# Optimization experiments

Hardware: AMD Instinct MI355X
Metric: run time of the kernel (lower is better)

## Reference

```python
import jax, jax.numpy as jnp
import numpy as np

N, E, HID, HEADS, EDIM = 32768, 262144, 64, 4, 3
C = HID  # per-head out channels (concat=False -> mean over heads)


def setup_inputs() -> dict:
    key = jax.random.key(0)
    ks = jax.random.split(key, 24)
    g = lambda k, shape, s=1.0: jax.random.normal(k, shape, jnp.float32) * s
    s_lin = 1.0 / np.sqrt(HID)
    s_edge = 1.0 / np.sqrt(EDIM)
    s_att = 1.0 / np.sqrt(C)
    inp = {
        "t": jnp.zeros((1,), jnp.float32),
        "h": g(ks[0], (N, HID)),
        "edge_index": jax.random.randint(ks[1], (2, E), 0, N, jnp.int32),
        "edge_attr": g(ks[2], (E, EDIM)),
        "W1": g(ks[3], (HID, HEADS * C), s_lin),
        "We1": g(ks[4], (EDIM, HEADS * C), s_edge),
        "att_src1": g(ks[5], (HEADS, C), s_att),
        "att_dst1": g(ks[6], (HEADS, C), s_att),
        "att_edge1": g(ks[7], (HEADS, C), s_att),
        "b1": jnp.zeros((C,), jnp.float32),
        "ln_g1": jnp.ones((HID,), jnp.float32),
        "ln_b1": jnp.zeros((HID,), jnp.float32),
        # last GAT layer's lin weight is scaled by 0.1 in __init__
        "W2": g(ks[8], (HID, HEADS * C), s_lin) * 0.1,
        "We2": g(ks[9], (EDIM, HEADS * C), s_edge),
        "att_src2": g(ks[10], (HEADS, C), s_att),
        "att_dst2": g(ks[11], (HEADS, C), s_att),
        "att_edge2": g(ks[12], (HEADS, C), s_att),
        "b2": jnp.zeros((C,), jnp.float32),
        "ln_g2": jnp.ones((HID,), jnp.float32),
        "ln_b2": jnp.zeros((HID,), jnp.float32),
    }
    return inp


def _gat_layer(z, src, dst, edge_attr, W, We, a_src, a_dst, a_edge, b):
    # PyG GATConv(edge_dim>0, concat=False, add_self_loops=False), eval mode (no dropout)
    x = (z @ W).reshape(-1, HEADS, C)                      # [N,H,C]
    alpha_s = jnp.einsum("nhc,hc->nh", x, a_src)           # [N,H]
    alpha_d = jnp.einsum("nhc,hc->nh", x, a_dst)           # [N,H]
    e = (edge_attr @ We).reshape(-1, HEADS, C)             # [E,H,C]
    alpha_e = jnp.einsum("ehc,hc->eh", e, a_edge)          # [E,H]
    logit = jax.nn.leaky_relu(alpha_s[src] + alpha_d[dst] + alpha_e, 0.2)  # [E,H]
    # segment softmax over incoming edges of each destination node
    m = jax.lax.stop_gradient(jax.ops.segment_max(logit, dst, num_segments=N))
    ex = jnp.exp(logit - m[dst])
    denom = jax.ops.segment_sum(ex, dst, num_segments=N)
    alpha = ex / (denom[dst] + 1e-16)                      # [E,H]
    msg = x[src] * alpha[..., None]                        # [E,H,C] gather + weight
    out = jax.ops.segment_sum(msg, dst, num_segments=N)    # [N,H,C] scatter-add
    return out.mean(axis=1) + b                            # head mean + bias -> [N,C]


def _layernorm(x, g, b, eps=1e-5):
    mu = x.mean(-1, keepdims=True)
    var = ((x - mu) ** 2).mean(-1, keepdims=True)
    return (x - mu) * jax.lax.rsqrt(var + eps) * g + b


def reference(t, h, edge_index, edge_attr, W1, We1, att_src1, att_dst1, att_edge1, b1,
              ln_g1, ln_b1, W2, We2, att_src2, att_dst2, att_edge2, b2, ln_g2, ln_b2):
    del t  # autonomous ODE func: t unused
    src, dst = edge_index[0], edge_index[1]
    z = h
    z = jax.nn.silu(_layernorm(_gat_layer(z, src, dst, edge_attr, W1, We1, att_src1, att_dst1, att_edge1, b1), ln_g1, ln_b1))
    z = jax.nn.silu(_layernorm(_gat_layer(z, src, dst, edge_attr, W2, We2, att_src2, att_dst2, att_edge2, b2), ln_g2, ln_b2))
    return z
```

## Files before the change

kernel.cpp:

```cpp
#include <hip/hip_runtime.h>
#include <math.h>

#define HIDDEN 64
#define HEADS 4
#define HC 256
#define CAP 64

typedef __attribute__((ext_vector_type(8))) short short8;
typedef __attribute__((ext_vector_type(4))) float f32x4;

__device__ __forceinline__ unsigned short f2bf(float f) {
    unsigned int u = __float_as_uint(f);
    u += 0x7fffu + ((u >> 16) & 1u);
    return (unsigned short)(u >> 16);
}

__global__ __launch_bounds__(256) void k_fused(const int* __restrict__ dst,
                                               const int* __restrict__ src,
                                               const float* __restrict__ ea,
                                               const float* __restrict__ h,
                                               const float* __restrict__ W1f,
                                               const float* __restrict__ W2f,
                                               const float* __restrict__ We1,
                                               const float* __restrict__ at1,
                                               const float* __restrict__ We2,
                                               const float* __restrict__ at2,
                                               int* __restrict__ counts,
                                               int* __restrict__ sb,
                                               float* __restrict__ eab,
                                               ushort* __restrict__ zb,
                                               ushort* __restrict__ wt1,
                                               ushort* __restrict__ wt2,
                                               float* __restrict__ wr, int E) {
    int t = threadIdx.x, b = blockIdx.x;
    if (b < 1024) {
        int e = b * 256 + t;
        if (e < E) {
            int d = dst[e];
            int c = atomicAdd(&counts[d], 1);
            if (c < CAP) {
                size_t slot = (size_t)d * CAP + c;
                sb[slot] = src[e];
                *(float4*)&eab[slot * 4] =
                    make_float4(ea[e * 3 + 0], ea[e * 3 + 1], ea[e * 3 + 2], 0.f);
            }
        }
    } else if (b < 3072) {
        int i = (b - 1024) * 256 + t;
        float4 v = ((const float4*)h)[i];
        ushort4 o;
        o.x = f2bf(v.x); o.y = f2bf(v.y); o.z = f2bf(v.z); o.w = f2bf(v.w);
        ((ushort4*)zb)[i] = o;
    } else if (b < 3136) {
        int j = (b - 3072) * 256 + t;
        int c = j >> 6, k = j & 63;
        wt1[j] = f2bf(W1f[k * HC + c]);
        wt2[j] = f2bf(W2f[k * HC + c]);
    } else {
        int wv = t >> 6, lane = t & 63;
#pragma unroll
        for (int it = 0; it < 6; ++it) {
            int comb = wv + it * 4;
            int layer = comb / 12;
            int dh = comb % 12;
            int d = dh >> 2, hh = dh & 3;
            const float* We = layer ? We2 : We1;
            const float* at = layer ? at2 : at1;
            float v = We[d * HC + hh * HIDDEN + lane] * at[hh * HIDDEN + lane];
            for (int o = 32; o > 0; o >>= 1) v += __shfl_down(v, o);
            if (lane == 0) wr[layer * 16 + d * HEADS + hh] = v;
        }
    }
}

__global__ __launch_bounds__(256) void k_tmfma(const ushort* __restrict__ zb,
                                               const ushort* __restrict__ wt,
                                               const float* __restrict__ asw,
                                               const float* __restrict__ adw,
                                               ushort* __restrict__ xb,
                                               float* __restrict__ as_,
                                               float* __restrict__ ad_) {
    int wave = threadIdx.x >> 6, lane = threadIdx.x & 63;
    int q = lane & 15, quad = lane >> 4;
    int row0 = blockIdx.x * 64 + wave * 16;

    const ushort* zrow = zb + (size_t)(row0 + q) * 64 + quad * 8;
    short8 a0 = *(const short8*)(zrow);
    short8 a1 = *(const short8*)(zrow + 32);

#pragma unroll
    for (int h = 0; h < 4; ++h) {
        float vs[4] = {0.f, 0.f, 0.f, 0.f};
        float vd[4] = {0.f, 0.f, 0.f, 0.f};
#pragma unroll
        for (int nt = 0; nt < 4; ++nt) {
            int col0 = h * 64 + nt * 16;
            const ushort* wrow = wt + (size_t)(col0 + q) * 64 + quad * 8;
            short8 b0 = *(const short8*)(wrow);
            short8 b1 = *(const short8*)(wrow + 32);
            f32x4 acc = {0.f, 0.f, 0.f, 0.f};
            acc = __builtin_amdgcn_mfma_f32_16x16x32_bf16(a0, b0, acc, 0, 0, 0);
            acc = __builtin_amdgcn_mfma_f32_16x16x32_bf16(a1, b1, acc, 0, 0, 0);
            int c = col0 + q;
            float aw = asw[c], dw = adw[c];
#pragma unroll
            for (int r = 0; r < 4; ++r) {
                float v = acc[r];
                xb[(size_t)(row0 + quad * 4 + r) * HC + c] = f2bf(v);
                vs[r] += v * aw;
                vd[r] += v * dw;
            }
        }
#pragma unroll
        for (int o = 1; o < 16; o <<= 1) {
#pragma unroll
            for (int r = 0; r < 4; ++r) {
                vs[r] += __shfl_xor(vs[r], o);
                vd[r] += __shfl_xor(vd[r], o);
            }
        }
        if (q < 4) {
            int n = row0 + quad * 4 + q;
            as_[n * 4 + h] = vs[q];
            ad_[n * 4 + h] = vd[q];
        }
    }
}

__global__ __launch_bounds__(256) void k_aggregate(
        const ushort* __restrict__ xb, const float* __restrict__ eab,
        const int* __restrict__ sb, const int* __restrict__ counts,
        const float* __restrict__ as_, const float* __restrict__ ad_,
        const float* __restrict__ wrl,
        const float* __restrict__ bias, const float* __restrict__ lng,
        const float* __restrict__ lnb, float* __restrict__ outf,
        ushort* __restrict__ outb, int N) {
    int lane = threadIdx.x & 63;
    int h = lane >> 4, sub = lane & 15;
    int e = sub & 1, g = sub >> 1;
    int wid = blockIdx.x * 4 + (threadIdx.x >> 6);
    int nwaves = gridDim.x * 4;

    float w0 = wrl[h], w1 = wrl[4 + h], w2 = wrl[8 + h];

    float bs[8], gm[8], bt[8];
#pragma unroll
    for (int k = 0; k < 8; ++k) {
        bs[k] = bias[g * 8 + k];
        gm[k] = lng[g * 8 + k];
        bt[k] = lnb[g * 8 + k];
    }

    for (int n = wid; n < N; n += nwaves) {
        int deg = counts[n];
        if (deg > CAP) deg = CAP;
        int base = n * CAP;
        float ad4 = ad_[n * 4 + h];

        float ssum = 0.f;
        float acc[8];
#pragma unroll
        for (int k = 0; k < 8; ++k) acc[k] = 0.f;

        for (int cs = 0; cs < deg; cs += 16) {
            int idx = cs + sub;
            int s_sub = 0;
            float wgt = 0.f;
            if (idx < deg) {
                s_sub = sb[base + idx];
                float4 av = *(const float4*)&eab[(size_t)(base + idx) * 4];
                float lg = as_[s_sub * 4 + h] + ad4
                         + av.x * w0 + av.y * w1 + av.z * w2;
                lg = (lg >= 0.f) ? lg : 0.2f * lg;
                wgt = __expf(lg);
            }
            ssum += wgt;

            int jb = deg - cs; if (jb > 16) jb = 16;
            for (int j4 = 0; j4 < jb; j4 += 4) {
                int sl0 = h * 16 + j4 + e;
                int sl1 = h * 16 + j4 + 2 + e;
                float q0 = __shfl(wgt, sl0);
                int s0 = __shfl(s_sub, sl0);
                float q1 = __shfl(wgt, sl1);
                int s1 = __shfl(s_sub, sl1);
                uint4 r0 = *(const uint4*)&xb[(size_t)s0 * HC + h * HIDDEN + g * 8];
                uint4 r1 = *(const uint4*)&xb[(size_t)s1 * HC + h * HIDDEN + g * 8];
                unsigned int u0[4] = {r0.x, r0.y, r0.z, r0.w};
                unsigned int u1[4] = {r1.x, r1.y, r1.z, r1.w};
#pragma unroll
                for (int k = 0; k < 4; ++k) {
                    acc[2 * k + 0] += q0 * __uint_as_float(u0[k] << 16);
                    acc[2 * k + 1] += q0 * __uint_as_float(u0[k] & 0xffff0000u);
                    acc[2 * k + 0] += q1 * __uint_as_float(u1[k] << 16);
                    acc[2 * k + 1] += q1 * __uint_as_float(u1[k] & 0xffff0000u);
                }
            }
        }
#pragma unroll
        for (int o = 1; o < 16; o <<= 1) ssum += __shfl_xor(ssum, o);
        float winv = 1.f / (ssum + 1e-16f);
#pragma unroll
        for (int k = 0; k < 8; ++k) acc[k] *= winv;
#pragma unroll
        for (int k = 0; k < 8; ++k) {
            acc[k] += __shfl_xor(acc[k], 1);
            acc[k] += __shfl_xor(acc[k], 16);
            acc[k] += __shfl_xor(acc[k], 32);
        }

        float u8[8], s1 = 0.f;
#pragma unroll
        for (int k = 0; k < 8; ++k) {
            u8[k] = acc[k] * 0.25f + bs[k];
            s1 += u8[k];
        }
#pragma unroll
        for (int o = 2; o < 16; o <<= 1) s1 += __shfl_xor(s1, o);
        float mu = s1 * (1.f / 64.f);
        float s2 = 0.f;
#pragma unroll
        for (int k = 0; k < 8; ++k) {
            float d = u8[k] - mu;
            s2 += d * d;
        }
#pragma unroll
        for (int o = 2; o < 16; o <<= 1) s2 += __shfl_xor(s2, o);
        float rstd = rsqrtf(s2 * (1.f / 64.f) + 1e-5f);
        float r[8];
#pragma unroll
        for (int k = 0; k < 8; ++k) {
            float y = (u8[k] - mu) * rstd * gm[k] + bt[k];
            r[k] = y / (1.f + __expf(-y));
        }
        if ((lane & 49) == 0) {
            if (outb) {
                uint4 pk;
                pk.x = (unsigned)f2bf(r[0]) | ((unsigned)f2bf(r[1]) << 16);
                pk.y = (unsigned)f2bf(r[2]) | ((unsigned)f2bf(r[3]) << 16);
                pk.z = (unsigned)f2bf(r[4]) | ((unsigned)f2bf(r[5]) << 16);
                pk.w = (unsigned)f2bf(r[6]) | ((unsigned)f2bf(r[7]) << 16);
                *(uint4*)&outb[(size_t)n * HIDDEN + g * 8] = pk;
            } else {
                float4* o4 = (float4*)&outf[(size_t)n * HIDDEN + g * 8];
                o4[0] = make_float4(r[0], r[1], r[2], r[3]);
                o4[1] = make_float4(r[4], r[5], r[6], r[7]);
            }
        }
    }
}


extern "C" void kernel_launch(void* const* d_in, const int* in_sizes, int n_in,
                              void* d_out, int out_size, void* d_ws, size_t ws_size,
                              hipStream_t stream) {
    const float* h   = (const float*)d_in[1];
    const int*   ei  = (const int*)d_in[2];
    const float* ea  = (const float*)d_in[3];
    const float* W1  = (const float*)d_in[4];
    const float* We1 = (const float*)d_in[5];
    const float* as1 = (const float*)d_in[6];
    const float* ad1 = (const float*)d_in[7];
    const float* ae1 = (const float*)d_in[8];
    const float* b1  = (const float*)d_in[9];
    const float* lg1 = (const float*)d_in[10];
    const float* lb1 = (const float*)d_in[11];
    const float* W2  = (const float*)d_in[12];
    const float* We2 = (const float*)d_in[13];
    const float* as2 = (const float*)d_in[14];
    const float* ad2 = (const float*)d_in[15];
    const float* ae2 = (const float*)d_in[16];
    const float* b2  = (const float*)d_in[17];
    const float* lg2 = (const float*)d_in[18];
    const float* lb2 = (const float*)d_in[19];

    const int N = in_sizes[1] / HIDDEN;
    const int E = in_sizes[2] / 2;
    const int* srcp = ei;
    const int* dstp = ei + E;

    char* w = (char*)d_ws;
    ushort* xb    = (ushort*)w; w += (size_t)N * HC * 2;
    ushort* zb    = (ushort*)w; w += (size_t)N * HIDDEN * 2;
    float* as_    = (float*)w;  w += (size_t)N * HEADS * 4;
    float* adv    = (float*)w;  w += (size_t)N * HEADS * 4;
    ushort* wt1   = (ushort*)w; w += 16384 * 2;
    ushort* wt2   = (ushort*)w; w += 16384 * 2;
    float* wr     = (float*)w;  w += 128;
    int* counts   = (int*)w;    w += (size_t)N * 4;
    int* sb       = (int*)w;    w += (size_t)N * CAP * 4;
    float* eab    = (float*)w;  w += (size_t)N * CAP * 4 * 4;

    hipMemsetAsync(counts, 0, (size_t)N * 4, stream);
    k_fused<<<3137, 256, 0, stream>>>(dstp, srcp, ea, h, W1, W2,
                                      We1, ae1, We2, ae2,
                                      counts, sb, eab, zb, wt1, wt2, wr, E);

    k_tmfma<<<N / 64, 256, 0, stream>>>(zb, wt1, as1, ad1, xb, as_, adv);
    k_aggregate<<<4096, 256, 0, stream>>>(xb, eab, sb, counts, as_, adv, wr,
                                          b1, lg1, lb1, nullptr, zb, N);
    k_tmfma<<<N / 64, 256, 0, stream>>>(zb, wt2, as2, ad2, xb, as_, adv);
    k_aggregate<<<4096, 256, 0, stream>>>(xb, eab, sb, counts, as_, adv, wr + 16,
                                          b2, lg2, lb2, (float*)d_out, nullptr, N);
}
```

Baseline: 221.6 us.

## Store edge attrs in bf16, transpose MFMA output, fully unroll aggregate gather

Bucketed edge attributes are stored as bf16 ushort4 instead of float4, halving that buffer's write and read traffic. The projection kernel swaps the MFMA operands so each lane holds four consecutive columns of one row. This allows vectorized ushort4 stores of x and float4 loads of the attention weights, and shrinks the attention-logit shuffle reduction. The aggregate inner loop is fully unrolled over 16 slots, with one gather per iteration instead of two. Slots past the degree get zero weight, but their loads still go to row 0 (src 0), which adds wasted gathers for low-degree nodes. Edge attributes also lose precision in bf16.

```diff
diff --git a/kernel.cpp b/kernel.cpp
--- a/kernel.cpp
+++ b/kernel.cpp
@@ -27,7 +27,7 @@
                                                const float* __restrict__ at2,
                                                int* __restrict__ counts,
                                                int* __restrict__ sb,
-                                               float* __restrict__ eab,
+                                               ushort* __restrict__ eab,
                                                ushort* __restrict__ zb,
                                                ushort* __restrict__ wt1,
                                                ushort* __restrict__ wt2,
@@ -41,8 +41,12 @@
             if (c < CAP) {
                 size_t slot = (size_t)d * CAP + c;
                 sb[slot] = src[e];
-                *(float4*)&eab[slot * 4] =
-                    make_float4(ea[e * 3 + 0], ea[e * 3 + 1], ea[e * 3 + 2], 0.f);
+                ushort4 ev;
+                ev.x = f2bf(ea[e * 3 + 0]);
+                ev.y = f2bf(ea[e * 3 + 1]);
+                ev.z = f2bf(ea[e * 3 + 2]);
+                ev.w = 0;
+                *(ushort4*)&eab[slot * 4] = ev;
             }
         }
     } else if (b < 3072) {
@@ -85,50 +89,41 @@
     int row0 = blockIdx.x * 64 + wave * 16;
 
     const ushort* zrow = zb + (size_t)(row0 + q) * 64 + quad * 8;
-    short8 a0 = *(const short8*)(zrow);
-    short8 a1 = *(const short8*)(zrow + 32);
+    short8 bz0 = *(const short8*)(zrow);
+    short8 bz1 = *(const short8*)(zrow + 32);
 
 #pragma unroll
     for (int h = 0; h < 4; ++h) {
-        float vs[4] = {0.f, 0.f, 0.f, 0.f};
-        float vd[4] = {0.f, 0.f, 0.f, 0.f};
+        float vs = 0.f, vd = 0.f;
 #pragma unroll
         for (int nt = 0; nt < 4; ++nt) {
             int col0 = h * 64 + nt * 16;
             const ushort* wrow = wt + (size_t)(col0 + q) * 64 + quad * 8;
-            short8 b0 = *(const short8*)(wrow);
-            short8 b1 = *(const short8*)(wrow + 32);
+            short8 aw0 = *(const short8*)(wrow);
+            short8 aw1 = *(const short8*)(wrow + 32);
             f32x4 acc = {0.f, 0.f, 0.f, 0.f};
-            acc = __builtin_amdgcn_mfma_f32_16x16x32_bf16(a0, b0, acc, 0, 0, 0);
-            acc = __builtin_amdgcn_mfma_f32_16x16x32_bf16(a1, b1, acc, 0, 0, 0);
-            int c = col0 + q;
-            float aw = asw[c], dw = adw[c];
-#pragma unroll
-            for (int r = 0; r < 4; ++r) {
-                float v = acc[r];
-                xb[(size_t)(row0 + quad * 4 + r) * HC + c] = f2bf(v);
-                vs[r] += v * aw;
-                vd[r] += v * dw;
-            }
-        }
-#pragma unroll
-        for (int o = 1; o < 16; o <<= 1) {
-#pragma unroll
-            for (int r = 0; r < 4; ++r) {
-                vs[r] += __shfl_xor(vs[r], o);
-                vd[r] += __shfl_xor(vd[r], o);
-            }
-        }
-        if (q < 4) {
-            int n = row0 + quad * 4 + q;
-            as_[n * 4 + h] = vs[q];
-            ad_[n * 4 + h] = vd[q];
+            acc = __builtin_amdgcn_mfma_f32_16x16x32_bf16(aw0, bz0, acc, 0, 0, 0);
+            acc = __builtin_amdgcn_mfma_f32_16x16x32_bf16(aw1, bz1, acc, 0, 0, 0);
+            float4 aw4 = *(const float4*)&asw[col0 + quad * 4];
+            float4 dw4 = *(const float4*)&adw[col0 + quad * 4];
+            ushort4 st;
+            st.x = f2bf(acc[0]); st.y = f2bf(acc[1]);
+            st.z = f2bf(acc[2]); st.w = f2bf(acc[3]);
+            *(ushort4*)&xb[(size_t)(row0 + q) * HC + col0 + quad * 4] = st;
+            vs += acc[0] * aw4.x + acc[1] * aw4.y + acc[2] * aw4.z + acc[3] * aw4.w;
+            vd += acc[0] * dw4.x + acc[1] * dw4.y + acc[2] * dw4.z + acc[3] * dw4.w;
+        }
+        vs += __shfl_xor(vs, 16); vs += __shfl_xor(vs, 32);
+        vd += __shfl_xor(vd, 16); vd += __shfl_xor(vd, 32);
+        if (quad == 0) {
+            as_[(row0 + q) * 4 + h] = vs;
+            ad_[(row0 + q) * 4 + h] = vd;
         }
     }
 }
 
 __global__ __launch_bounds__(256) void k_aggregate(
-        const ushort* __restrict__ xb, const float* __restrict__ eab,
+        const ushort* __restrict__ xb, const ushort* __restrict__ eab,
         const int* __restrict__ sb, const int* __restrict__ counts,
         const float* __restrict__ as_, const float* __restrict__ ad_,
         const float* __restrict__ wrl,
@@ -168,32 +163,27 @@
             float wgt = 0.f;
             if (idx < deg) {
                 s_sub = sb[base + idx];
-                float4 av = *(const float4*)&eab[(size_t)(base + idx) * 4];
-                float lg = as_[s_sub * 4 + h] + ad4
-                         + av.x * w0 + av.y * w1 + av.z * w2;
+                ushort4 ev = *(const ushort4*)&eab[(size_t)(base + idx) * 4];
+                float a0 = __uint_as_float((unsigned)ev.x << 16);
+                float a1 = __uint_as_float((unsigned)ev.y << 16);
+                float a2 = __uint_as_float((unsigned)ev.z << 16);
+                float lg = as_[s_sub * 4 + h] + ad4 + a0 * w0 + a1 * w1 + a2 * w2;
                 lg = (lg >= 0.f) ? lg : 0.2f * lg;
                 wgt = __expf(lg);
             }
             ssum += wgt;
 
-            int jb = deg - cs; if (jb > 16) jb = 16;
-            for (int j4 = 0; j4 < jb; j4 += 4) {
-                int sl0 = h * 16 + j4 + e;
-                int sl1 = h * 16 + j4 + 2 + e;
-                float q0 = __shfl(wgt, sl0);
-                int s0 = __shfl(s_sub, sl0);
-                float q1 = __shfl(wgt, sl1);
-                int s1 = __shfl(s_sub, sl1);
-                uint4 r0 = *(const uint4*)&xb[(size_t)s0 * HC + h * HIDDEN + g * 8];
-                uint4 r1 = *(const uint4*)&xb[(size_t)s1 * HC + h * HIDDEN + g * 8];
-                unsigned int u0[4] = {r0.x, r0.y, r0.z, r0.w};
-                unsigned int u1[4] = {r1.x, r1.y, r1.z, r1.w};
+#pragma unroll
+            for (int j2 = 0; j2 < 16; j2 += 2) {
+                int sl = h * 16 + j2 + e;
+                float wj = __shfl(wgt, sl);
+                int sj = __shfl(s_sub, sl);
+                uint4 raw = *(const uint4*)&xb[(size_t)sj * HC + h * HIDDEN + g * 8];
+                unsigned int u[4] = {raw.x, raw.y, raw.z, raw.w};
 #pragma unroll
                 for (int k = 0; k < 4; ++k) {
-                    acc[2 * k + 0] += q0 * __uint_as_float(u0[k] << 16);
-                    acc[2 * k + 1] += q0 * __uint_as_float(u0[k] & 0xffff0000u);
-                    acc[2 * k + 0] += q1 * __uint_as_float(u1[k] << 16);
-                    acc[2 * k + 1] += q1 * __uint_as_float(u1[k] & 0xffff0000u);
+                    acc[2 * k + 0] += wj * __uint_as_float(u[k] << 16);
+                    acc[2 * k + 1] += wj * __uint_as_float(u[k] & 0xffff0000u);
                 }
             }
         }
@@ -289,7 +279,7 @@
     float* wr     = (float*)w;  w += 128;
     int* counts   = (int*)w;    w += (size_t)N * 4;
     int* sb       = (int*)w;    w += (size_t)N * CAP * 4;
-    float* eab    = (float*)w;  w += (size_t)N * CAP * 4 * 4;
+    ushort* eab   = (ushort*)w; w += (size_t)N * CAP * 4 * 2;
 
     hipMemsetAsync(counts, 0, (size_t)N * 4, stream);
     k_fused<<<3137, 256, 0, stream>>>(dstp, srcp, ea, h, W1, W2,
```

Measured after the change: 246.3 us. 11.1% more time.
